# Kernel optimization log

Measured on AMD Instinct MI355X. Metric: run time of the kernel, lower is better.

Reference implementation:

```python
import jax, jax.numpy as jnp
import numpy as np
import math

HIDDEN = 1024
N_HEADS = 16
HEAD_DIM = HIDDEN // N_HEADS  # 64
B, S = 4, 8192


def setup_inputs() -> dict:
    key = jax.random.key(0)
    ks = jax.random.split(key, 5)
    scale = 1.0 / math.sqrt(HIDDEN)
    return {
        "hidden_states": jax.random.normal(ks[0], (B, S, HIDDEN), dtype=jnp.float32),
        "Wq": jax.random.normal(ks[1], (HIDDEN, HIDDEN), dtype=jnp.float32) * scale,
        "Wk": jax.random.normal(ks[2], (HIDDEN, HIDDEN), dtype=jnp.float32) * scale,
        "Wv": jax.random.normal(ks[3], (HIDDEN, HIDDEN), dtype=jnp.float32) * scale,
        "Wo": jax.random.normal(ks[4], (HIDDEN, HIDDEN), dtype=jnp.float32) * scale,
    }


def reference(hidden_states, Wq, Wk, Wv, Wo):
    b, s, _ = hidden_states.shape
    # nn.Linear(bias=False): y = x @ W.T
    q = (hidden_states @ Wq.T).reshape(b, s, N_HEADS, HEAD_DIM)
    k = (hidden_states @ Wk.T).reshape(b, s, N_HEADS, HEAD_DIM)
    v = (hidden_states @ Wv.T).reshape(b, s, N_HEADS, HEAD_DIM)
    # Faithful to source: NO transpose to (b,h,s,d); matmul contracts head_dim
    # per (batch, position), yielding [b, s, h, h] head-mixing weights.
    attn = jnp.einsum("bshd,bstd->bsht", q, k) / math.sqrt(HEAD_DIM)
    attn = jax.nn.softmax(attn, axis=-1)
    out = jnp.einsum("bsht,bstd->bshd", attn, v).reshape(b, s, HIDDEN)
    return out @ Wo.T
```

## Files before the change

kernel.cpp:

```cpp
#include <hip/hip_runtime.h>
#include <hip/hip_bf16.h>


typedef short bf16x8 __attribute__((ext_vector_type(8)));
typedef float f32x4  __attribute__((ext_vector_type(4)));

__device__ __forceinline__ float bf2f(short u) {
    union { unsigned int ui; float f; } cv;
    cv.ui = ((unsigned int)(unsigned short)u) << 16;
    return cv.f;
}
__device__ __forceinline__ short f2bf(float f) {
    __hip_bfloat16 h = __float2bfloat16(f);
    return *reinterpret_cast<short*>(&h);
}

__device__ __forceinline__ void gload_lds16(const void* g, void* lds) {
    const unsigned __attribute__((address_space(1)))* gp =
        reinterpret_cast<const unsigned __attribute__((address_space(1)))*>((unsigned long long)g);
    unsigned __attribute__((address_space(3)))* lp =
        reinterpret_cast<unsigned __attribute__((address_space(3)))*>(
            (unsigned int)(unsigned long long)lds);
    __builtin_amdgcn_global_load_lds(gp, lp, 16, 0, 0);
}

__global__ void detect_dtype(const unsigned* __restrict__ x, int* __restrict__ flag) {
    __shared__ int cnt;
    if (threadIdx.x == 0) cnt = 0;
    __syncthreads();
    int c = 0;
    for (int i = threadIdx.x; i < 4096; i += 256) {
        const unsigned u = x[(long)i * 4001 + 3];
        const unsigned b = (u >> 7) & 0xFF;
        c += (b >= 0x70 && b <= 0x87) ? 1 : 0;
    }
    atomicAdd(&cnt, c);
    __syncthreads();
    if (threadIdx.x == 0) *flag = (cnt > 2048) ? 0 : 1;
}

__global__ void convert_all(const void* __restrict__ X,
                            const void* __restrict__ W0, const void* __restrict__ W1,
                            const void* __restrict__ W2, const void* __restrict__ W3,
                            short* __restrict__ dst, long total,
                            const int* __restrict__ flag) {
    constexpr long WELEM = 1024 * 1024;
    const int f = *flag;
    const long step = (long)gridDim.x * blockDim.x * 8;
    for (long i = ((long)blockIdx.x * blockDim.x + threadIdx.x) * 8; i < total; i += step) {
        const void* src;
        long off;
        if (i < 4 * WELEM) {
            const int w = (int)(i >> 20);
            src = (w == 0) ? W0 : (w == 1) ? W1 : (w == 2) ? W2 : W3;
            off = i & (WELEM - 1);
        } else {
            src = X;
            off = i - 4 * WELEM;
        }
        if (f) {
            const float* s = (const float*)src + off;
            const f32x4 a = *(const f32x4*)s;
            const f32x4 b = *(const f32x4*)(s + 4);
            bf16x8 o;
            o[0] = f2bf(a[0]); o[1] = f2bf(a[1]); o[2] = f2bf(a[2]); o[3] = f2bf(a[3]);
            o[4] = f2bf(b[0]); o[5] = f2bf(b[1]); o[6] = f2bf(b[2]); o[7] = f2bf(b[3]);
            *(bf16x8*)(dst + i) = o;
        } else {
            *(bf16x8*)(dst + i) = *(const bf16x8*)((const short*)src + off);
        }
    }
}

__device__ __forceinline__ void gemm256_core8(const short* __restrict__ A,
                                              const short* __restrict__ W,
                                              void* __restrict__ C,
                                              const int* flag_fp32,
                                              long m0, int n0, short* lds) {
    constexpr int K = 1024, N = 1024;
    const int tid  = threadIdx.x;
    const int lane = tid & 63;
    const int wid  = tid >> 6;
    const int wm = wid >> 2, wn = wid & 3;

    short* A0 = lds;
    short* B0 = lds + 16384;
    short* A1 = lds + 32768;
    short* B1 = lds + 49152;

    const int srl = tid >> 3;
    const int kcs = (tid & 7) ^ (srl & 7);
    int aoff[4], boff[4];
    #pragma unroll
    for (int i = 0; i < 4; ++i) {
        const int row = i * 64 + srl;
        aoff[i] = (int)((m0 + row) * K + kcs * 8);
        boff[i] = (n0 + row) * K + kcs * 8;
    }
    const int ldsw = wid * 512;

    f32x4 acc[8][4] = {};

    #pragma unroll
    for (int i = 0; i < 4; ++i) gload_lds16(A + aoff[i], A0 + i * 4096 + ldsw);
    #pragma unroll
    for (int i = 0; i < 4; ++i) gload_lds16(W + boff[i], B0 + i * 4096 + ldsw);
    asm volatile("s_waitcnt vmcnt(0)" ::: "memory");
    __builtin_amdgcn_s_barrier();

    for (int t = 0; t < 16; ++t) {
        const int cur = t & 1;
        const short* rA = cur ? A1 : A0;
        const short* rB = cur ? B1 : B0;
        short* sA = cur ? A0 : A1;
        short* sB = cur ? B0 : B1;
        const int kadd = (t + 1) * 64;
        const bool more = (t < 15);

        #pragma unroll
        for (int ks = 0; ks < 2; ++ks) {
            const int kx8 = ((ks * 4 + (lane >> 4)) ^ (lane & 7)) * 8;
            bf16x8 af[8], bfr[4];
            #pragma unroll
            for (int m = 0; m < 8; ++m)
                af[m] = *(const bf16x8*)(rA + ((wm * 128 + m * 16 + (lane & 15)) * 64) + kx8);
            #pragma unroll
            for (int n = 0; n < 4; ++n)
                bfr[n] = *(const bf16x8*)(rB + ((wn * 64 + n * 16 + (lane & 15)) * 64) + kx8);
            __builtin_amdgcn_sched_barrier(0);
            __builtin_amdgcn_s_barrier();
            __builtin_amdgcn_sched_barrier(0);
            if (more) {
                if (ks == 0) {
                    #pragma unroll
                    for (int i = 0; i < 4; ++i)
                        gload_lds16(A + aoff[i] + kadd, sA + i * 4096 + ldsw);
                } else {
                    #pragma unroll
                    for (int i = 0; i < 4; ++i)
                        gload_lds16(W + boff[i] + kadd, sB + i * 4096 + ldsw);
                }
            }
            asm volatile("s_waitcnt lgkmcnt(0)" ::: "memory");
            __builtin_amdgcn_sched_barrier(0);
            __builtin_amdgcn_s_setprio(1);
            #pragma unroll
            for (int m = 0; m < 8; ++m)
                #pragma unroll
                for (int n = 0; n < 4; ++n)
                    acc[m][n] = __builtin_amdgcn_mfma_f32_16x16x32_bf16(
                                    af[m], bfr[n], acc[m][n], 0, 0, 0);
            __builtin_amdgcn_s_setprio(0);
            __builtin_amdgcn_sched_barrier(0);
            if (ks == 1) {
                asm volatile("s_waitcnt vmcnt(0)" ::: "memory");
                __builtin_amdgcn_s_barrier();
            }
        }
    }

    const int f = flag_fp32 ? *flag_fp32 : 0;
    #pragma unroll
    for (int mf = 0; mf < 8; ++mf) {
        #pragma unroll
        for (int nf = 0; nf < 4; ++nf) {
            const int  col   = n0 + wn * 64 + nf * 16 + (lane & 15);
            const long rbase = m0 + wm * 128 + mf * 16 + (lane >> 4) * 4;
            if (f) {
                float* Cf = (float*)C;
                #pragma unroll
                for (int r = 0; r < 4; ++r)
                    Cf[(rbase + r) * N + col] = acc[mf][nf][r];
            } else {
                short* Cs = (short*)C;
                #pragma unroll
                for (int r = 0; r < 4; ++r)
                    Cs[(rbase + r) * N + col] = f2bf(acc[mf][nf][r]);
            }
        }
    }
}

__device__ __forceinline__ void gemm256_core4(const short* __restrict__ A,
                                              const short* __restrict__ W,
                                              void* __restrict__ C,
                                              const int* flag_fp32,
                                              long m0, int n0, short* lds) {
    constexpr int K = 1024, N = 1024;
    const int tid  = threadIdx.x;
    const int lane = tid & 63;
    const int wid  = tid >> 6;
    const int wm = wid >> 1, wn = wid & 1;

    short* A0 = lds;
    short* B0 = lds + 16384;
    short* A1 = lds + 32768;
    short* B1 = lds + 49152;

    const int srl = tid >> 3;
    const int kcs = (tid & 7) ^ (srl & 7);
    int aoff[8], boff[8];
    #pragma unroll
    for (int i = 0; i < 8; ++i) {
        const int row = i * 32 + srl;
        aoff[i] = (int)((m0 + row) * K + kcs * 8);
        boff[i] = (n0 + row) * K + kcs * 8;
    }
    const int ldsw = wid * 512;

    f32x4 acc[8][8] = {};

    #pragma unroll
    for (int i = 0; i < 8; ++i) gload_lds16(A + aoff[i], A0 + i * 2048 + ldsw);
    #pragma unroll
    for (int i = 0; i < 8; ++i) gload_lds16(W + boff[i], B0 + i * 2048 + ldsw);
    asm volatile("s_waitcnt vmcnt(0)" ::: "memory");
    __builtin_amdgcn_s_barrier();

    const int arow = wm * 128 + (lane & 15);
    const int brow = wn * 128 + (lane & 15);

    for (int t = 0; t < 16; ++t) {
        const int cur = t & 1;
        const short* rA = cur ? A1 : A0;
        const short* rB = cur ? B1 : B0;
        short* sA = cur ? A0 : A1;
        short* sB = cur ? B0 : B1;
        const int kadd = (t + 1) * 64;
        const bool more = (t < 15);

        #pragma unroll
        for (int ks = 0; ks < 2; ++ks) {
            const int kx8 = ((ks * 4 + (lane >> 4)) ^ (lane & 7)) * 8;
            bf16x8 af[8], bfr[8];
            #pragma unroll
            for (int m = 0; m < 8; ++m)
                af[m] = *(const bf16x8*)(rA + ((arow + m * 16) * 64) + kx8);
            #pragma unroll
            for (int n = 0; n < 8; ++n)
                bfr[n] = *(const bf16x8*)(rB + ((brow + n * 16) * 64) + kx8);
            __builtin_amdgcn_sched_barrier(0);
            __builtin_amdgcn_s_barrier();
            __builtin_amdgcn_sched_barrier(0);
            if (more) {
                if (ks == 0) {
                    #pragma unroll
                    for (int i = 0; i < 8; ++i)
                        gload_lds16(A + aoff[i] + kadd, sA + i * 2048 + ldsw);
                } else {
                    #pragma unroll
                    for (int i = 0; i < 8; ++i)
                        gload_lds16(W + boff[i] + kadd, sB + i * 2048 + ldsw);
                }
            }
            asm volatile("s_waitcnt lgkmcnt(0)" ::: "memory");
            __builtin_amdgcn_sched_barrier(0);
            __builtin_amdgcn_s_setprio(1);
            #pragma unroll
            for (int m = 0; m < 8; ++m)
                #pragma unroll
                for (int n = 0; n < 8; ++n)
                    acc[m][n] = __builtin_amdgcn_mfma_f32_16x16x32_bf16(
                                    af[m], bfr[n], acc[m][n], 0, 0, 0);
            __builtin_amdgcn_s_setprio(0);
            __builtin_amdgcn_sched_barrier(0);
            if (ks == 1) {
                asm volatile("s_waitcnt vmcnt(0)" ::: "memory");
                __builtin_amdgcn_s_barrier();
            }
        }
    }

    const int f = flag_fp32 ? *flag_fp32 : 0;
    #pragma unroll
    for (int mf = 0; mf < 8; ++mf) {
        #pragma unroll
        for (int nf = 0; nf < 8; ++nf) {
            const int  col   = n0 + wn * 128 + nf * 16 + (lane & 15);
            const long rbase = m0 + wm * 128 + mf * 16 + (lane >> 4) * 4;
            if (f) {
                float* Cf = (float*)C;
                #pragma unroll
                for (int r = 0; r < 4; ++r)
                    Cf[(rbase + r) * N + col] = acc[mf][nf][r];
            } else {
                short* Cs = (short*)C;
                #pragma unroll
                for (int r = 0; r < 4; ++r)
                    Cs[(rbase + r) * N + col] = f2bf(acc[mf][nf][r]);
            }
        }
    }
}

__global__ __launch_bounds__(512, 2) void gemm_qkv256(const short* __restrict__ A,
                                                      const short* __restrict__ W0,
                                                      const short* __restrict__ W1,
                                                      const short* __restrict__ W2,
                                                      short* __restrict__ C0,
                                                      short* __restrict__ C1,
                                                      short* __restrict__ C2) {
    __shared__ __align__(16) short lds[65536];
    const int nwg = gridDim.x;
    const int q8  = nwg >> 3;
    const int d   = blockIdx.x;
    const int lin = (d & 7) * q8 + (d >> 3);
    const int x   = lin / 12;
    const int r   = lin - x * 12;
    const int yy  = r / 3;
    const int z   = r - yy * 3;
    const short* W = (z == 0) ? W0 : (z == 1) ? W1 : W2;
    short*       C = (z == 0) ? C0 : (z == 1) ? C1 : C2;
    gemm256_core8(A, W, C, nullptr, (long)x * 256, yy * 256, lds);
}

__global__ __launch_bounds__(256, 1) void gemm_out256(const short* __restrict__ A,
                                                      const short* __restrict__ W,
                                                      void* __restrict__ C,
                                                      long moff,
                                                      const int* __restrict__ flag) {
    __shared__ __align__(16) short lds[65536];
    const int nwg = gridDim.x;
    const int q8  = nwg >> 3;
    const int d   = blockIdx.x;
    const int lin = (d & 7) * q8 + (d >> 3);
    const int x   = lin >> 2;
    const int yy  = lin & 3;
    gemm256_core4(A, W, C, flag, moff + (long)x * 256, yy * 256, lds);
}

__global__ __launch_bounds__(256) void attn_mix(const short* __restrict__ Q,
                                                const short* __restrict__ K,
                                                const short* __restrict__ V,
                                                short* __restrict__ Z) {
    constexpr int RS = 72;
    __shared__ short sq[4][16 * RS];
    __shared__ short sk[4][16 * RS];
    __shared__ short sv[4][16 * RS];
    __shared__ float sp[4][256];

    const int  tid  = threadIdx.x;
    const int  lane = tid & 63;
    const int  w    = tid >> 6;
    const long tok  = (long)blockIdx.x * 4 + w;

    const short* qg = Q + tok * 1024;
    const short* kg = K + tok * 1024;
    const short* vg = V + tok * 1024;

    #pragma unroll
    for (int it = 0; it < 2; ++it) {
        const int c   = lane + 64 * it;
        const int row = c >> 3;
        const int cc  = (c & 7) * 8;
        *(bf16x8*)&sq[w][row * RS + cc] = *(const bf16x8*)(qg + c * 8);
        *(bf16x8*)&sk[w][row * RS + cc] = *(const bf16x8*)(kg + c * 8);
        *(bf16x8*)&sv[w][row * RS + cc] = *(const bf16x8*)(vg + c * 8);
    }
    __syncthreads();

    const int h  = lane >> 2;
    const int t0 = (lane & 3) * 4;
    float sc[4] = {0.f, 0.f, 0.f, 0.f};
    for (int d = 0; d < 64; ++d) {
        const float qv = bf2f(sq[w][h * RS + d]);
        #pragma unroll
        for (int j = 0; j < 4; ++j)
            sc[j] += qv * bf2f(sk[w][(t0 + j) * RS + d]);
    }
    #pragma unroll
    for (int j = 0; j < 4; ++j) sc[j] *= 0.125f;

    float mx = fmaxf(fmaxf(sc[0], sc[1]), fmaxf(sc[2], sc[3]));
    mx = fmaxf(mx, __shfl_xor(mx, 1));
    mx = fmaxf(mx, __shfl_xor(mx, 2));
    float ex[4], s = 0.f;
    #pragma unroll
    for (int j = 0; j < 4; ++j) { ex[j] = __expf(sc[j] - mx); s += ex[j]; }
    s += __shfl_xor(s, 1);
    s += __shfl_xor(s, 2);
    const float inv = 1.f / s;
    #pragma unroll
    for (int j = 0; j < 4; ++j) sp[w][h * 16 + t0 + j] = ex[j] * inv;
    __syncthreads();

    const int dbase = (lane & 3) * 16;
    float o[16] = {};
    for (int t = 0; t < 16; ++t) {
        const float p = sp[w][h * 16 + t];
        const bf16x8 v0 = *(const bf16x8*)&sv[w][t * RS + dbase];
        const bf16x8 v1 = *(const bf16x8*)&sv[w][t * RS + dbase + 8];
        #pragma unroll
        for (int e = 0; e < 8; ++e) {
            o[e]     += p * bf2f(v0[e]);
            o[e + 8] += p * bf2f(v1[e]);
        }
    }
    bf16x8 ov0, ov1;
    #pragma unroll
    for (int e = 0; e < 8; ++e) { ov0[e] = f2bf(o[e]); ov1[e] = f2bf(o[e + 8]); }
    *(bf16x8*)(Z + tok * 1024 + lane * 16)     = ov0;
    *(bf16x8*)(Z + tok * 1024 + lane * 16 + 8) = ov1;
}

extern "C" void kernel_launch(void* const* d_in, const int* in_sizes, int n_in,
                              void* d_out, int out_size, void* d_ws, size_t ws_size,
                              hipStream_t stream) {
    const void* X = d_in[0];

    const long TOT = 32768;
    constexpr long WELEM = 1024 * 1024;

    char* ws   = (char*)d_ws;
    int*  flag = (int*)ws;
    short* Wqb = (short*)(ws + 256);
    short* Wkb = Wqb + WELEM;
    short* Wvb = Wkb + WELEM;
    short* Wob = Wvb + WELEM;
    short* dyn = Wob + WELEM;

    const size_t fixed = 256 + 4 * WELEM * 2;
    long chunk = 256;
    const long tiers[4] = {32768, 8192, 2048, 512};
    for (int i = 0; i < 4; ++i)
        if (fixed + (size_t)6 * tiers[i] * 1024 * 2 <= ws_size) { chunk = tiers[i]; break; }

    short* Xb = dyn;
    short* Qb = Xb + chunk * 1024;
    short* Kb = Qb + chunk * 1024;
    short* Vb = Kb + chunk * 1024;
    short* Zb = Vb + chunk * 1024;

    detect_dtype<<<1, 256, 0, stream>>>((const unsigned*)X, flag);

    if (chunk == TOT) {
        convert_all<<<2048, 256, 0, stream>>>(X, d_in[1], d_in[2], d_in[3], d_in[4],
                                              Wqb, 4 * WELEM + TOT * 1024, flag);
        gemm_qkv256<<<dim3((TOT / 256) * 12), 512, 0, stream>>>(Xb, Wqb, Wkb, Wvb,
                                                                Qb, Kb, Vb);
        attn_mix<<<dim3(TOT / 4), 256, 0, stream>>>(Qb, Kb, Vb, Zb);
        gemm_out256<<<dim3((TOT / 256) * 4), 256, 0, stream>>>(Zb, Wob, d_out, 0, flag);
    } else {
        convert_all<<<512, 256, 0, stream>>>(X, d_in[1], d_in[2], d_in[3], d_in[4],
                                             Wqb, 4 * WELEM, flag);
        for (long t0 = 0; t0 < TOT; t0 += chunk) {
            convert_all<<<2048, 256, 0, stream>>>(
                (const void*)((const char*)X + (size_t)t0 * 1024 * 4),
                d_in[1], d_in[2], d_in[3], d_in[4],
                Xb - 4 * WELEM, 4 * WELEM + chunk * 1024, flag);
            gemm_qkv256<<<dim3((chunk / 256) * 12), 512, 0, stream>>>(Xb, Wqb, Wkb, Wvb,
                                                                      Qb, Kb, Vb);
            attn_mix<<<dim3(chunk / 4), 256, 0, stream>>>(Qb, Kb, Vb, Zb);
            gemm_out256<<<dim3((chunk / 256) * 4), 256, 0, stream>>>(Zb - t0 * 1024, Wob,
                                                                     d_out, t0, flag);
        }
    }
}
```

Before: 405.8 us.

## Fuse fp32-to-bf16 input conversion into QKV GEMM A-tile loading

The QKV GEMM now reads the fp32 hidden states directly. In the fp32 case it converts A tiles to bf16 in registers and writes them to LDS, replacing the async global-to-LDS copy, with the next tile's loads software-pipelined across the two k-substeps. This removes the separate conversion pass over X and the bf16 copy of X in the workspace, which also lets larger chunks fit. In exchange, A traffic per tile is twice as wide, and the loads now go through VGPRs with conversion ALU work inside the main loop, which may add latency and register pressure.

```diff
diff --git a/kernel.cpp b/kernel.cpp
--- a/kernel.cpp
+++ b/kernel.cpp
@@ -72,16 +72,21 @@
     }
 }
 
-__device__ __forceinline__ void gemm256_core8(const short* __restrict__ A,
+__device__ __forceinline__ void gemm256_core8(const void* __restrict__ Asrc,
                                               const short* __restrict__ W,
                                               void* __restrict__ C,
-                                              const int* flag_fp32,
+                                              const int* out_f32,
+                                              const int* a_f32,
+                                              long arow_off,
                                               long m0, int n0, short* lds) {
     constexpr int K = 1024, N = 1024;
     const int tid  = threadIdx.x;
     const int lane = tid & 63;
     const int wid  = tid >> 6;
     const int wm = wid >> 2, wn = wid & 3;
+    const int af32 = a_f32 ? *a_f32 : 0;
+    const short* Ab = (const short*)Asrc;
+    const float* Af = (const float*)Asrc;
 
     short* A0 = lds;
     short* B0 = lds + 16384;
@@ -94,18 +99,34 @@
     #pragma unroll
     for (int i = 0; i < 4; ++i) {
         const int row = i * 64 + srl;
-        aoff[i] = (int)((m0 + row) * K + kcs * 8);
+        aoff[i] = (int)((arow_off + m0 + row) * K + kcs * 8);
         boff[i] = (n0 + row) * K + kcs * 8;
     }
     const int ldsw = wid * 512;
+    const int tslot = tid << 3;
 
     f32x4 acc[8][4] = {};
 
-    #pragma unroll
-    for (int i = 0; i < 4; ++i) gload_lds16(A + aoff[i], A0 + i * 4096 + ldsw);
-    #pragma unroll
-    for (int i = 0; i < 4; ++i) gload_lds16(W + boff[i], B0 + i * 4096 + ldsw);
-    asm volatile("s_waitcnt vmcnt(0)" ::: "memory");
+    if (af32) {
+        #pragma unroll
+        for (int u = 0; u < 4; ++u) {
+            const float* s = Af + aoff[u];
+            const f32x4 lo = *(const f32x4*)s;
+            const f32x4 hi = *(const f32x4*)(s + 4);
+            bf16x8 o;
+            o[0] = f2bf(lo[0]); o[1] = f2bf(lo[1]); o[2] = f2bf(lo[2]); o[3] = f2bf(lo[3]);
+            o[4] = f2bf(hi[0]); o[5] = f2bf(hi[1]); o[6] = f2bf(hi[2]); o[7] = f2bf(hi[3]);
+            *(bf16x8*)(A0 + u * 4096 + tslot) = o;
+        }
+    } else {
+        #pragma unroll
+        for (int u = 0; u < 4; ++u)
+            gload_lds16(Ab + aoff[u], A0 + u * 4096 + ldsw);
+    }
+    #pragma unroll
+    for (int u = 0; u < 4; ++u)
+        gload_lds16(W + boff[u], B0 + u * 4096 + ldsw);
+    asm volatile("s_waitcnt vmcnt(0) lgkmcnt(0)" ::: "memory");
     __builtin_amdgcn_s_barrier();
 
     for (int t = 0; t < 16; ++t) {
@@ -117,9 +138,15 @@
         const int kadd = (t + 1) * 64;
         const bool more = (t < 15);
 
-        #pragma unroll
-        for (int ks = 0; ks < 2; ++ks) {
-            const int kx8 = ((ks * 4 + (lane >> 4)) ^ (lane & 7)) * 8;
+        f32x4 a0lo, a0hi, a1lo, a1hi;
+        if (more && af32) {
+            const float* s0 = Af + aoff[0] + kadd;
+            a0lo = *(const f32x4*)s0; a0hi = *(const f32x4*)(s0 + 4);
+            const float* s1 = Af + aoff[1] + kadd;
+            a1lo = *(const f32x4*)s1; a1hi = *(const f32x4*)(s1 + 4);
+        }
+        {
+            const int kx8 = (((lane >> 4)) ^ (lane & 7)) * 8;
             bf16x8 af[8], bfr[4];
             #pragma unroll
             for (int m = 0; m < 8; ++m)
@@ -130,16 +157,10 @@
             __builtin_amdgcn_sched_barrier(0);
             __builtin_amdgcn_s_barrier();
             __builtin_amdgcn_sched_barrier(0);
-            if (more) {
-                if (ks == 0) {
-                    #pragma unroll
-                    for (int i = 0; i < 4; ++i)
-                        gload_lds16(A + aoff[i] + kadd, sA + i * 4096 + ldsw);
-                } else {
-                    #pragma unroll
-                    for (int i = 0; i < 4; ++i)
-                        gload_lds16(W + boff[i] + kadd, sB + i * 4096 + ldsw);
-                }
+            if (more && !af32) {
+                #pragma unroll
+                for (int u = 0; u < 4; ++u)
+                    gload_lds16(Ab + aoff[u] + kadd, sA + u * 4096 + ldsw);
             }
             asm volatile("s_waitcnt lgkmcnt(0)" ::: "memory");
             __builtin_amdgcn_sched_barrier(0);
@@ -152,14 +173,79 @@
                                     af[m], bfr[n], acc[m][n], 0, 0, 0);
             __builtin_amdgcn_s_setprio(0);
             __builtin_amdgcn_sched_barrier(0);
-            if (ks == 1) {
+        }
+
+        {
+            const int kx8 = ((4 + (lane >> 4)) ^ (lane & 7)) * 8;
+            bf16x8 af[8], bfr[4];
+            #pragma unroll
+            for (int m = 0; m < 8; ++m)
+                af[m] = *(const bf16x8*)(rA + ((wm * 128 + m * 16 + (lane & 15)) * 64) + kx8);
+            #pragma unroll
+            for (int n = 0; n < 4; ++n)
+                bfr[n] = *(const bf16x8*)(rB + ((wn * 64 + n * 16 + (lane & 15)) * 64) + kx8);
+            __builtin_amdgcn_sched_barrier(0);
+            __builtin_amdgcn_s_barrier();
+            __builtin_amdgcn_sched_barrier(0);
+            f32x4 a2lo, a2hi, a3lo, a3hi;
+            if (more && af32) {
+                {
+                    bf16x8 o;
+                    o[0] = f2bf(a0lo[0]); o[1] = f2bf(a0lo[1]); o[2] = f2bf(a0lo[2]); o[3] = f2bf(a0lo[3]);
+                    o[4] = f2bf(a0hi[0]); o[5] = f2bf(a0hi[1]); o[6] = f2bf(a0hi[2]); o[7] = f2bf(a0hi[3]);
+                    *(bf16x8*)(sA + 0 * 4096 + tslot) = o;
+                }
+                {
+                    bf16x8 o;
+                    o[0] = f2bf(a1lo[0]); o[1] = f2bf(a1lo[1]); o[2] = f2bf(a1lo[2]); o[3] = f2bf(a1lo[3]);
+                    o[4] = f2bf(a1hi[0]); o[5] = f2bf(a1hi[1]); o[6] = f2bf(a1hi[2]); o[7] = f2bf(a1hi[3]);
+                    *(bf16x8*)(sA + 1 * 4096 + tslot) = o;
+                }
+                const float* s2 = Af + aoff[2] + kadd;
+                a2lo = *(const f32x4*)s2; a2hi = *(const f32x4*)(s2 + 4);
+                const float* s3 = Af + aoff[3] + kadd;
+                a3lo = *(const f32x4*)s3; a3hi = *(const f32x4*)(s3 + 4);
+            }
+            if (more) {
+                #pragma unroll
+                for (int u = 0; u < 4; ++u)
+                    gload_lds16(W + boff[u] + kadd, sB + u * 4096 + ldsw);
+            }
+            asm volatile("s_waitcnt lgkmcnt(0)" ::: "memory");
+            __builtin_amdgcn_sched_barrier(0);
+            __builtin_amdgcn_s_setprio(1);
+            #pragma unroll
+            for (int m = 0; m < 8; ++m)
+                #pragma unroll
+                for (int n = 0; n < 4; ++n)
+                    acc[m][n] = __builtin_amdgcn_mfma_f32_16x16x32_bf16(
+                                    af[m], bfr[n], acc[m][n], 0, 0, 0);
+            __builtin_amdgcn_s_setprio(0);
+            __builtin_amdgcn_sched_barrier(0);
+            if (more && af32) {
+                {
+                    bf16x8 o;
+                    o[0] = f2bf(a2lo[0]); o[1] = f2bf(a2lo[1]); o[2] = f2bf(a2lo[2]); o[3] = f2bf(a2lo[3]);
+                    o[4] = f2bf(a2hi[0]); o[5] = f2bf(a2hi[1]); o[6] = f2bf(a2hi[2]); o[7] = f2bf(a2hi[3]);
+                    *(bf16x8*)(sA + 2 * 4096 + tslot) = o;
+                }
+                {
+                    bf16x8 o;
+                    o[0] = f2bf(a3lo[0]); o[1] = f2bf(a3lo[1]); o[2] = f2bf(a3lo[2]); o[3] = f2bf(a3lo[3]);
+                    o[4] = f2bf(a3hi[0]); o[5] = f2bf(a3hi[1]); o[6] = f2bf(a3hi[2]); o[7] = f2bf(a3hi[3]);
+                    *(bf16x8*)(sA + 3 * 4096 + tslot) = o;
+                }
+                asm volatile("s_waitcnt lgkmcnt(0)" ::: "memory");
+                __builtin_amdgcn_sched_barrier(0);
+            }
+            if (more) {
                 asm volatile("s_waitcnt vmcnt(0)" ::: "memory");
                 __builtin_amdgcn_s_barrier();
             }
         }
     }
 
-    const int f = flag_fp32 ? *flag_fp32 : 0;
+    const int f = out_f32 ? *out_f32 : 0;
     #pragma unroll
     for (int mf = 0; mf < 8; ++mf) {
         #pragma unroll
@@ -293,13 +379,15 @@
     }
 }
 
-__global__ __launch_bounds__(512, 2) void gemm_qkv256(const short* __restrict__ A,
+__global__ __launch_bounds__(512, 2) void gemm_qkv256(const void* __restrict__ X,
                                                       const short* __restrict__ W0,
                                                       const short* __restrict__ W1,
                                                       const short* __restrict__ W2,
                                                       short* __restrict__ C0,
                                                       short* __restrict__ C1,
-                                                      short* __restrict__ C2) {
+                                                      short* __restrict__ C2,
+                                                      const int* __restrict__ flag,
+                                                      long arow_off) {
     __shared__ __align__(16) short lds[65536];
     const int nwg = gridDim.x;
     const int q8  = nwg >> 3;
@@ -311,7 +399,7 @@
     const int z   = r - yy * 3;
     const short* W = (z == 0) ? W0 : (z == 1) ? W1 : W2;
     short*       C = (z == 0) ? C0 : (z == 1) ? C1 : C2;
-    gemm256_core8(A, W, C, nullptr, (long)x * 256, yy * 256, lds);
+    gemm256_core8(X, W, C, nullptr, flag, arow_off, (long)x * 256, yy * 256, lds);
 }
 
 __global__ __launch_bounds__(256, 1) void gemm_out256(const short* __restrict__ A,
@@ -423,36 +511,22 @@
     long chunk = 256;
     const long tiers[4] = {32768, 8192, 2048, 512};
     for (int i = 0; i < 4; ++i)
-        if (fixed + (size_t)6 * tiers[i] * 1024 * 2 <= ws_size) { chunk = tiers[i]; break; }
-
-    short* Xb = dyn;
-    short* Qb = Xb + chunk * 1024;
+        if (fixed + (size_t)8 * tiers[i] * 1024 <= ws_size) { chunk = tiers[i]; break; }
+
+    short* Qb = dyn;
     short* Kb = Qb + chunk * 1024;
     short* Vb = Kb + chunk * 1024;
     short* Zb = Vb + chunk * 1024;
 
     detect_dtype<<<1, 256, 0, stream>>>((const unsigned*)X, flag);
-
-    if (chunk == TOT) {
-        convert_all<<<2048, 256, 0, stream>>>(X, d_in[1], d_in[2], d_in[3], d_in[4],
-                                              Wqb, 4 * WELEM + TOT * 1024, flag);
-        gemm_qkv256<<<dim3((TOT / 256) * 12), 512, 0, stream>>>(Xb, Wqb, Wkb, Wvb,
-                                                                Qb, Kb, Vb);
-        attn_mix<<<dim3(TOT / 4), 256, 0, stream>>>(Qb, Kb, Vb, Zb);
-        gemm_out256<<<dim3((TOT / 256) * 4), 256, 0, stream>>>(Zb, Wob, d_out, 0, flag);
-    } else {
-        convert_all<<<512, 256, 0, stream>>>(X, d_in[1], d_in[2], d_in[3], d_in[4],
-                                             Wqb, 4 * WELEM, flag);
-        for (long t0 = 0; t0 < TOT; t0 += chunk) {
-            convert_all<<<2048, 256, 0, stream>>>(
-                (const void*)((const char*)X + (size_t)t0 * 1024 * 4),
-                d_in[1], d_in[2], d_in[3], d_in[4],
-                Xb - 4 * WELEM, 4 * WELEM + chunk * 1024, flag);
-            gemm_qkv256<<<dim3((chunk / 256) * 12), 512, 0, stream>>>(Xb, Wqb, Wkb, Wvb,
-                                                                      Qb, Kb, Vb);
-            attn_mix<<<dim3(chunk / 4), 256, 0, stream>>>(Qb, Kb, Vb, Zb);
-            gemm_out256<<<dim3((chunk / 256) * 4), 256, 0, stream>>>(Zb - t0 * 1024, Wob,
-                                                                     d_out, t0, flag);
-        }
-    }
-}
+    convert_all<<<512, 256, 0, stream>>>(X, d_in[1], d_in[2], d_in[3], d_in[4],
+                                         Wqb, 4 * WELEM, flag);
+
+    for (long t0 = 0; t0 < TOT; t0 += chunk) {
+        gemm_qkv256<<<dim3((chunk / 256) * 12), 512, 0, stream>>>(
+            X, Wqb, Wkb, Wvb, Qb, Kb, Vb, flag, t0);
+        attn_mix<<<dim3(chunk / 4), 256, 0, stream>>>(Qb, Kb, Vb, Zb);
+        gemm_out256<<<dim3((chunk / 256) * 4), 256, 0, stream>>>(
+            Zb - t0 * 1024, Wob, d_out, t0, flag);
+    }
+}
```

Result: slower. 435.7 us (+7.4%).
